# Optimization experiments

Hardware: AMD Instinct MI355X
Metric: run time of the kernel (lower is better)

Reference implementation:

```python
import jax, jax.numpy as jnp
import numpy as np
import math

INC, OUTC, NPARAM = 64, 128, 8
B, D, H, W = 2, 12, 48, 48
BN_EPS = 1e-5


def _p_n(num_param):
    # replicates LDConv_3D._get_p_n kernel-point layout
    base = round(math.sqrt(num_param))
    dep = round(num_param ** (1.0 / 3.0))
    row = num_param // (base * dep)
    mod = num_param % (base * dep)
    z, x, y = np.meshgrid(np.arange(dep), np.arange(row), np.arange(base), indexing='ij')
    z, x, y = z.ravel(), x.ravel(), y.ravel()
    if mod > 0:
        mz, mx, my = np.meshgrid(np.arange(dep, dep + 1), np.arange(row, row + 1), np.arange(mod), indexing='ij')
        z = np.concatenate([z, mz.ravel()])
        x = np.concatenate([x, mx.ravel()])
        y = np.concatenate([y, my.ravel()])
    return (jnp.asarray(z, jnp.float32), jnp.asarray(x, jnp.float32), jnp.asarray(y, jnp.float32))


def _conv3d(x, w, stride, pad):
    return jax.lax.conv_general_dilated(x, w, window_strides=stride, padding=pad,
                                        dimension_numbers=('NCDHW', 'OIDHW', 'NCDHW'))


def setup_inputs() -> dict:
    key = jax.random.key(0)
    ks = jax.random.split(key, 5)
    x = jax.random.normal(ks[0], (B, INC, D, H, W), jnp.float32)
    w_p = jax.random.normal(ks[1], (3 * NPARAM, INC, 3, 3, 3), jnp.float32) * 0.01
    b_p = jax.random.normal(ks[2], (3 * NPARAM,), jnp.float32) * 0.01
    w_conv = jax.random.normal(ks[3], (OUTC, INC, NPARAM, 1, 1), jnp.float32) * (1.0 / math.sqrt(INC * NPARAM))
    gamma = jnp.ones((OUTC,), jnp.float32)
    beta = jnp.zeros((OUTC,), jnp.float32)
    return {'x': x, 'w_p': w_p, 'b_p': b_p, 'w_conv': w_conv, 'gamma': gamma, 'beta': beta}


def reference(x, w_p, b_p, w_conv, gamma, beta):
    b, c, d, h, w = x.shape
    N = NPARAM
    # learned offsets: (b, 3N, d, h, w)
    offset = _conv3d(x, w_p, (1, 1, 1), [(1, 1), (1, 1), (1, 1)]) + b_p[None, :, None, None, None]
    off = jnp.transpose(offset, (0, 2, 3, 4, 1))  # b d h w 3N
    oz, ox, oy = off[..., :N], off[..., N:2 * N], off[..., 2 * N:]
    pnz, pnx, pny = _p_n(N)
    # sampling positions p = p_0 + p_n + offset  (stride=1)
    pz = oz + jnp.arange(d, dtype=jnp.float32)[None, :, None, None, None] + pnz
    px = ox + jnp.arange(h, dtype=jnp.float32)[None, None, :, None, None] + pnx
    py = oy + jnp.arange(w, dtype=jnp.float32)[None, None, None, :, None] + pny
    # integer corner coords (detached floor, clamped)
    fz = jnp.floor(jax.lax.stop_gradient(pz))
    fx = jnp.floor(jax.lax.stop_gradient(px))
    fy = jnp.floor(jax.lax.stop_gradient(py))
    qltz = jnp.clip(fz, 0, d - 1)
    qltx = jnp.clip(fx, 0, h - 1)
    qlty = jnp.clip(fy, 0, w - 1)
    qrbz = jnp.clip(fz + 1, 0, d - 1)
    qrbx = jnp.clip(fx + 1, 0, h - 1)
    qrby = jnp.clip(fy + 1, 0, w - 1)
    # clamped continuous positions
    pzc = jnp.clip(pz, 0, d - 1)
    pxc = jnp.clip(px, 0, h - 1)
    pyc = jnp.clip(py, 0, w - 1)
    # trilinear weights for the 4 gathered corners (as in source)
    g_lt = (1 + (qltz - pzc)) * (1 + (qltx - pxc)) * (1 + (qlty - pyc))
    g_rb = (1 - (qrbz - pzc)) * (1 - (qrbx - pxc)) * (1 - (qrby - pyc))
    g_lb = (1 + (qltz - pzc)) * (1 - (qrbx - pxc)) * (1 + (qlty - pyc))
    g_rt = (1 - (qrbz - pzc)) * (1 + (qltx - pxc)) * (1 - (qrby - pyc))
    x_flat = x.reshape(b, c, d * h * w)
    def gath(qz, qx, qy):
        idx = (qz.astype(jnp.int32) * (h * w) + qx.astype(jnp.int32) * w + qy.astype(jnp.int32)).reshape(b, -1)
        g = jax.vmap(lambda xf, i: jnp.take(xf, i, axis=1))(x_flat, idx)
        return g.reshape(b, c, d, h, w, N)
    x_lt = gath(qltz, qltx, qlty)
    x_rb = gath(qrbz, qrbx, qrby)
    x_lb = gath(qltz, qrbx, qlty)
    x_rt = gath(qrbz, qltx, qrby)
    x_off = (g_lt[:, None] * x_lt + g_rb[:, None] * x_rb +
             g_lb[:, None] * x_lb + g_rt[:, None] * x_rt)  # b c d h w N
    # rearrange 'b c d h w n -> b c (d n) h w'
    x_off = jnp.transpose(x_off, (0, 1, 2, 5, 3, 4)).reshape(b, c, d * N, h, w)
    out = _conv3d(x_off, w_conv, (N, 1, 1), [(0, 0), (0, 0), (0, 0)])  # b outc d h w
    # BatchNorm3d (training-mode batch stats, biased var) + SiLU
    mean = jnp.mean(out, axis=(0, 2, 3, 4), keepdims=True)
    var = jnp.mean((out - mean) ** 2, axis=(0, 2, 3, 4), keepdims=True)
    out = (out - mean) * jax.lax.rsqrt(var + BN_EPS)
    out = out * gamma[None, :, None, None, None] + beta[None, :, None, None, None]
    return jax.nn.silu(out)
```

## Files before the change

### kernel.cpp

```cpp
#include <hip/hip_runtime.h>
#include <math.h>

#define BATCH 2
#define INC   64
#define OUTCH 128
#define NP    8
#define DD    12
#define HH    48
#define WW    48
#define HW    (HH*WW)
#define DHW   (DD*HW)
#define SPTS  (BATCH*DHW)
#define KDIM  (INC*NP)
#define NELEM (BATCH*OUTCH*DHW)
#define VSTRIDE 520

#define WS_W2B  0
#define WS_W3   32768
#define WS_PART 88064
#define WS_XT   90112
#define WS_OFF  1859584

typedef __attribute__((ext_vector_type(8))) short short8;
typedef __attribute__((ext_vector_type(4))) float floatx4;

__device__ __forceinline__ ushort f2bf(float f) {
    unsigned u = __float_as_uint(f);
    unsigned r = (u + 0x7fffu + ((u >> 16) & 1u)) >> 16;
    return (ushort)r;
}

__device__ __forceinline__ unsigned interp2(unsigned a, unsigned b, unsigned c, unsigned d,
                                            float g0, float g1, float g2, float g3) {
    float vl = g0 * __uint_as_float(a << 16) + g1 * __uint_as_float(b << 16)
             + g2 * __uint_as_float(c << 16) + g3 * __uint_as_float(d << 16);
    float vh = g0 * __uint_as_float(a & 0xffff0000u) + g1 * __uint_as_float(b & 0xffff0000u)
             + g2 * __uint_as_float(c & 0xffff0000u) + g3 * __uint_as_float(d & 0xffff0000u);
    return (unsigned)f2bf(vl) | ((unsigned)f2bf(vh) << 16);
}

__global__ __launch_bounds__(256) void k_prep_w2b(const float* __restrict__ wc,
                                                  ushort* __restrict__ w2b) {
    int t = blockIdx.x * 256 + threadIdx.x;
    int j  = t & 7;
    int oc = (t >> 3) & 127;
    int kq = t >> 10;
    int e  = kq * 8 + j;
    int ic = e & 63;
    int n  = e >> 6;
    w2b[t] = f2bf(wc[(oc * INC + ic) * NP + n]);
}

__global__ __launch_bounds__(256) void k_prep_w3(const float* __restrict__ wp,
                                                 float* __restrict__ w3c) {
    int t = blockIdx.x * 256 + threadIdx.x;
    int ch = t & 31;
    int iu = t >> 5;
    w3c[t] = (ch < 24) ? wp[ch * 1728 + iu] : 0.f;
}

__global__ __launch_bounds__(256) void k_transpose_x(const float* __restrict__ x,
                                                     unsigned* __restrict__ xTu) {
    int t = blockIdx.x * 256 + threadIdx.x;
    int icp = t & 31;
    int sg  = t >> 5;
    int b   = sg / DHW;
    int s   = sg - b * DHW;
    const float* xb = x + (size_t)b * INC * DHW + s;
    float v0 = xb[(2 * icp) * DHW];
    float v1 = xb[(2 * icp + 1) * DHW];
    xTu[t] = (unsigned)f2bf(v0) | ((unsigned)f2bf(v1) << 16);
}

__global__ __launch_bounds__(256, 4) void k_conv(const float* __restrict__ x,
                                                 const float* __restrict__ w3c,
                                                 const float* __restrict__ bp,
                                                 float* __restrict__ off) {
    int t    = threadIdx.x;
    int lane = t & 63;
    int hgq  = __builtin_amdgcn_readfirstlane(t >> 6);
    int q0 = blockIdx.x * 128;
    int bb = q0 / DHW;
    int s0 = q0 - bb * DHW;
    int dp = s0 / HW;
    int rp = s0 - dp * HW + 2 * lane;
    int hp = rp / WW;
    int c0 = rp - hp * WW;
    const float* xb = x + (size_t)bb * INC * DHW;
    const float* wbase = w3c + hgq * 6;

    int rAo = (hp > 0      ? hp - 1 : 0     ) * WW;
    int rMo = hp * WW;
    int rBo = (hp < HH - 1 ? hp + 1 : HH - 1) * WW;
    int oL = (c0 > 0)  ? c0 - 2 : 0;
    int oM = c0;
    int oR = (c0 < 46) ? c0 + 2 : 46;

    float rm0 = (hp > 0)      ? 1.f : 0.f;
    float rm2 = (hp < HH - 1) ? 1.f : 0.f;
    float clm = (c0 > 0)      ? 1.f : 0.f;
    float crm = (c0 < 46)     ? 1.f : 0.f;
    float m0[9], m1[9];
    #pragma unroll
    for (int kx = 0; kx < 3; ++kx) {
        float rmv = kx == 0 ? rm0 : (kx == 1 ? 1.f : rm2);
        #pragma unroll
        for (int ky = 0; ky < 3; ++ky) {
            int u = kx * 3 + ky;
            m0[u] = rmv * (ky == 0 ? clm : 1.f);
            m1[u] = rmv * (ky == 2 ? crm : 1.f);
        }
    }

    float acc[2][6];
    #pragma unroll
    for (int c = 0; c < 6; ++c) { acc[0][c] = bp[hgq * 6 + c]; acc[1][c] = bp[hgq * 6 + c]; }

    #pragma unroll 1
    for (int kz = 0; kz < 3; ++kz) {
        int z = dp + kz - 1;
        if ((unsigned)z >= DD) continue;
        const float* xz = xb + z * HW;
        #pragma unroll 2
        for (int ic = 0; ic < 64; ++ic) {
            const float* xp = xz + (size_t)ic * DHW;
            float2 LA = *reinterpret_cast<const float2*>(xp + rAo + oL);
            float2 MA = *reinterpret_cast<const float2*>(xp + rAo + oM);
            float2 RA = *reinterpret_cast<const float2*>(xp + rAo + oR);
            float2 LM = *reinterpret_cast<const float2*>(xp + rMo + oL);
            float2 MM = *reinterpret_cast<const float2*>(xp + rMo + oM);
            float2 RM = *reinterpret_cast<const float2*>(xp + rMo + oR);
            float2 LB = *reinterpret_cast<const float2*>(xp + rBo + oL);
            float2 MB = *reinterpret_cast<const float2*>(xp + rBo + oM);
            float2 RB = *reinterpret_cast<const float2*>(xp + rBo + oR);
            const float* wk = wbase + (ic * 27 + kz * 9) * 32;
            #pragma unroll
            for (int kx = 0; kx < 3; ++kx) {
                float tv[4];
                if (kx == 0)      { tv[0] = LA.y; tv[1] = MA.x; tv[2] = MA.y; tv[3] = RA.x; }
                else if (kx == 1) { tv[0] = LM.y; tv[1] = MM.x; tv[2] = MM.y; tv[3] = RM.x; }
                else              { tv[0] = LB.y; tv[1] = MB.x; tv[2] = MB.y; tv[3] = RB.x; }
                #pragma unroll
                for (int ky = 0; ky < 3; ++ky) {
                    int u = kx * 3 + ky;
                    const float* w6 = wk + u * 32;
                    float xv0 = tv[ky]     * m0[u];
                    float xv1 = tv[ky + 1] * m1[u];
                    #pragma unroll
                    for (int c = 0; c < 6; ++c) {
                        acc[0][c] = fmaf(xv0, w6[c], acc[0][c]);
                        acc[1][c] = fmaf(xv1, w6[c], acc[1][c]);
                    }
                }
            }
        }
    }

    float2* o0 = reinterpret_cast<float2*>(off + (size_t)(q0 + 2 * lane) * 24 + hgq * 6);
    o0[0] = make_float2(acc[0][0], acc[0][1]);
    o0[1] = make_float2(acc[0][2], acc[0][3]);
    o0[2] = make_float2(acc[0][4], acc[0][5]);
    float2* o1 = reinterpret_cast<float2*>(off + (size_t)(q0 + 2 * lane + 1) * 24 + hgq * 6);
    o1[0] = make_float2(acc[1][0], acc[1][1]);
    o1[1] = make_float2(acc[1][2], acc[1][3]);
    o1[2] = make_float2(acc[1][4], acc[1][5]);
}

__global__ __launch_bounds__(256, 4) void k_fused(const unsigned* __restrict__ xTu,
                                                  const float* __restrict__ off,
                                                  const ushort* __restrict__ w2b,
                                                  float* __restrict__ out) {
    __shared__ __align__(16) ushort sVb[32 * VSTRIDE];
    __shared__ int   sMi[4][256];
    __shared__ float sMg[4][256];
    __shared__ __align__(16) unsigned stgBuf[64 * 36];

    int t  = threadIdx.x;
    int q0 = blockIdx.x * 32;
    int bb = q0 / DHW;

    {
        int i = t >> 3, n = t & 7;
        int s = q0 + i - bb * DHW;
        int d = s / HW; int r = s - d * HW; int h = r / WW; int w = r - h * WW;

        const float* op = off + (size_t)(q0 + i) * 24;
        float a0 = op[n];
        float a1 = op[8 + n];
        float a2 = op[16 + n];

        float pnz = (n < 6) ? (float)(n / 3) : 2.f;
        float pnx = (n < 6) ? 0.f : 1.f;
        float pny = (n < 6) ? (float)(n % 3) : (float)(n - 6);
        float pz = a0 + (float)d + pnz;
        float px = a1 + (float)h + pnx;
        float py = a2 + (float)w + pny;
        float fz = floorf(pz), fx = floorf(px), fy = floorf(py);
        float z0 = fminf(fmaxf(fz, 0.f), DD - 1.f), z1 = fminf(fmaxf(fz + 1.f, 0.f), DD - 1.f);
        float x0 = fminf(fmaxf(fx, 0.f), HH - 1.f), x1 = fminf(fmaxf(fx + 1.f, 0.f), HH - 1.f);
        float y0 = fminf(fmaxf(fy, 0.f), WW - 1.f), y1 = fminf(fmaxf(fy + 1.f, 0.f), WW - 1.f);
        float pzc = fminf(fmaxf(pz, 0.f), DD - 1.f);
        float pxc = fminf(fmaxf(px, 0.f), HH - 1.f);
        float pyc = fminf(fmaxf(py, 0.f), WW - 1.f);
        float wz0 = 1.f + z0 - pzc, wz1 = 1.f - z1 + pzc;
        float wx0 = 1.f + x0 - pxc, wx1 = 1.f - x1 + pxc;
        float wy0 = 1.f + y0 - pyc, wy1 = 1.f - y1 + pyc;
        float c0 = wz0 * wy0, c1 = wz1 * wy1;
        int iz0 = (int)z0, iz1 = (int)z1, ix0 = (int)x0, ix1 = (int)x1, iy0 = (int)y0, iy1 = (int)y1;
        sMi[0][t] = (iz0 * HH + ix0) * WW + iy0;
        sMi[1][t] = (iz0 * HH + ix1) * WW + iy0;
        sMi[2][t] = (iz1 * HH + ix0) * WW + iy1;
        sMi[3][t] = (iz1 * HH + ix1) * WW + iy1;
        sMg[0][t] = c0 * wx0;
        sMg[1][t] = c0 * wx1;
        sMg[2][t] = c1 * wx0;
        sMg[3][t] = c1 * wx1;
    }
    __syncthreads();

    {
        const unsigned* xTb = xTu + (size_t)bb * DHW * 32;
        unsigned* sVbU = reinterpret_cast<unsigned*>(sVb);
        int c  = t >> 3, o = t & 7;
        int tk = t >> 4, chq = t & 15;

        #pragma unroll 1
        for (int cc = 0; cc < 16; ++cc) {
            #pragma unroll
            for (int r2 = 0; r2 < 2; ++r2) {
                int cl  = r2 * 32 + c;
                int gt  = cc * 16 + (cl >> 2);
                int cid = cl & 3;
                int idx = sMi[cid][gt];
                uint4 v = reinterpret_cast<const uint4*>(xTb + (size_t)idx * 32)[o];
                *reinterpret_cast<uint4*>(&stgBuf[cl * 36 + o * 4]) = v;
            }
            __syncthreads();
            {
                int gt = cc * 16 + tk;
                float g0 = sMg[0][gt], g1 = sMg[1][gt], g2 = sMg[2][gt], g3 = sMg[3][gt];
                uint2 A = *reinterpret_cast<const uint2*>(&stgBuf[(tk * 4 + 0) * 36 + chq * 2]);
                uint2 B = *reinterpret_cast<const uint2*>(&stgBuf[(tk * 4 + 1) * 36 + chq * 2]);
                uint2 C = *reinterpret_cast<const uint2*>(&stgBuf[(tk * 4 + 2) * 36 + chq * 2]);
                uint2 D = *reinterpret_cast<const uint2*>(&stgBuf[(tk * 4 + 3) * 36 + chq * 2]);
                unsigned o0 = interp2(A.x, B.x, C.x, D.x, g0, g1, g2, g3);
                unsigned o1 = interp2(A.y, B.y, C.y, D.y, g0, g1, g2, g3);
                int ii = gt >> 3, nn = gt & 7;
                int wb = ii * (VSTRIDE / 2) + nn * 32 + chq * 2;
                sVbU[wb]     = o0;
                sVbU[wb + 1] = o1;
            }
            __syncthreads();
        }
    }

    {
        int lane = t & 63;
        int wid  = t >> 6;
        int l16  = lane & 15;
        int q    = lane >> 4;
        int ocA0 = (wid * 2) * 16 + l16;
        const ushort* A0 = w2b + ((q * 128) + ocA0) * 8;
        const ushort* A1 = A0 + 16 * 8;
        const ushort* B0 = sVb + l16 * VSTRIDE + q * 8;
        const ushort* B1 = B0 + 16 * VSTRIDE;

        floatx4 c00 = {0.f, 0.f, 0.f, 0.f};
        floatx4 c01 = {0.f, 0.f, 0.f, 0.f};
        floatx4 c10 = {0.f, 0.f, 0.f, 0.f};
        floatx4 c11 = {0.f, 0.f, 0.f, 0.f};

        #pragma unroll 4
        for (int kt = 0; kt < 16; ++kt) {
            short8 af0 = *reinterpret_cast<const short8*>(A0 + kt * 4096);
            short8 af1 = *reinterpret_cast<const short8*>(A1 + kt * 4096);
            short8 bf0 = *reinterpret_cast<const short8*>(B0 + kt * 32);
            short8 bf1 = *reinterpret_cast<const short8*>(B1 + kt * 32);
            c00 = __builtin_amdgcn_mfma_f32_16x16x32_bf16(af0, bf0, c00, 0, 0, 0);
            c01 = __builtin_amdgcn_mfma_f32_16x16x32_bf16(af0, bf1, c01, 0, 0, 0);
            c10 = __builtin_amdgcn_mfma_f32_16x16x32_bf16(af1, bf0, c10, 0, 0, 0);
            c11 = __builtin_amdgcn_mfma_f32_16x16x32_bf16(af1, bf1, c11, 0, 0, 0);
        }

        int s0 = q0 - bb * DHW;
        float* outb = out + (size_t)bb * OUTCH * DHW + s0;
        int ocRow = (wid * 2) * 16 + q * 4;
        #pragma unroll
        for (int rg = 0; rg < 4; ++rg) {
            outb[(ocRow + rg) * DHW + l16]            = c00[rg];
            outb[(ocRow + rg) * DHW + 16 + l16]       = c01[rg];
            outb[(ocRow + 16 + rg) * DHW + l16]       = c10[rg];
            outb[(ocRow + 16 + rg) * DHW + 16 + l16]  = c11[rg];
        }
    }
}

__global__ __launch_bounds__(256) void k_stats_partial(const float* __restrict__ out,
                                                       float* __restrict__ part) {
    int c = blockIdx.x >> 3;
    int j = blockIdx.x & 7;
    int b = j & 1, quarter = j >> 1;
    const float4* p = reinterpret_cast<const float4*>(
        out + (size_t)(b * OUTCH + c) * DHW + quarter * (DHW / 4));
    float sum = 0.f, ss = 0.f;
    for (int s = threadIdx.x; s < DHW / 16; s += 256) {
        float4 v = p[s];
        sum += v.x + v.y + v.z + v.w;
        ss = fmaf(v.x, v.x, ss); ss = fmaf(v.y, v.y, ss);
        ss = fmaf(v.z, v.z, ss); ss = fmaf(v.w, v.w, ss);
    }
    __shared__ float r1[256], r2[256];
    r1[threadIdx.x] = sum; r2[threadIdx.x] = ss;
    __syncthreads();
    for (int ofs = 128; ofs > 0; ofs >>= 1) {
        if (threadIdx.x < ofs) {
            r1[threadIdx.x] += r1[threadIdx.x + ofs];
            r2[threadIdx.x] += r2[threadIdx.x + ofs];
        }
        __syncthreads();
    }
    if (threadIdx.x == 0) {
        part[c * 8 + j]             = r1[0];
        part[OUTCH * 8 + c * 8 + j] = r2[0];
    }
}

__global__ __launch_bounds__(256) void k_bn_silu(float* __restrict__ out,
                                                 const float* __restrict__ part,
                                                 const float* __restrict__ gamma,
                                                 const float* __restrict__ beta) {
    int t = blockIdx.x * 256 + threadIdx.x;
    int base = t * 4;
    int c = (base / DHW) & 127;
    float sum = 0.f, ss = 0.f;
    #pragma unroll
    for (int j = 0; j < 8; ++j) {
        sum += part[c * 8 + j];
        ss  += part[OUTCH * 8 + c * 8 + j];
    }
    const float inv_n = 1.f / (float)(BATCH * DHW);
    float mean = sum * inv_n;
    float var  = ss * inv_n - mean * mean;
    float sc   = gamma[c] * rsqrtf(var + 1e-5f);
    float bi   = beta[c] - mean * sc;
    float4 v = *reinterpret_cast<float4*>(&out[base]);
    float y0 = fmaf(v.x, sc, bi);
    float y1 = fmaf(v.y, sc, bi);
    float y2 = fmaf(v.z, sc, bi);
    float y3 = fmaf(v.w, sc, bi);
    v.x = y0 / (1.f + expf(-y0));
    v.y = y1 / (1.f + expf(-y1));
    v.z = y2 / (1.f + expf(-y2));
    v.w = y3 / (1.f + expf(-y3));
    *reinterpret_cast<float4*>(&out[base]) = v;
}

extern "C" void kernel_launch(void* const* d_in, const int* in_sizes, int n_in,
                              void* d_out, int out_size, void* d_ws, size_t ws_size,
                              hipStream_t stream) {
    const float* x     = (const float*)d_in[0];
    const float* wp    = (const float*)d_in[1];
    const float* bp    = (const float*)d_in[2];
    const float* wc    = (const float*)d_in[3];
    const float* gamma = (const float*)d_in[4];
    const float* beta  = (const float*)d_in[5];
    float* out = (float*)d_out;
    float* ws  = (float*)d_ws;

    ushort*   w2b  = reinterpret_cast<ushort*>(ws + WS_W2B);
    float*    w3c  = ws + WS_W3;
    float*    part = ws + WS_PART;
    unsigned* xTu  = reinterpret_cast<unsigned*>(ws + WS_XT);
    float*    off  = ws + WS_OFF;

    k_prep_w2b<<<65536 / 256, 256, 0, stream>>>(wc, w2b);
    k_prep_w3<<<55296 / 256, 256, 0, stream>>>(wp, w3c);
    k_conv<<<SPTS / 128, 256, 0, stream>>>(x, w3c, bp, off);
    k_transpose_x<<<(SPTS * 32) / 256, 256, 0, stream>>>(x, xTu);
    k_fused<<<SPTS / 32, 256, 0, stream>>>(xTu, off, w2b, out);
    k_stats_partial<<<OUTCH * 8, 256, 0, stream>>>(out, part);
    k_bn_silu<<<(NELEM / 4) / 256, 256, 0, stream>>>(out, part, gamma, beta);
}
```

Measured before the change: 257.8 us.

## Transpose input to channel-last fp32 for offset conv and vectorize channel loads

A single transpose kernel now writes both a channel-last fp32 copy of x (placed in the output buffer as scratch) and the packed bf16 copy used by the fused kernel. The offset conv reads four channels at a time with float4 loads from the channel-last layout instead of strided per-channel float2 loads, and its launch bound is relaxed to 2 blocks per CU. The aim is fewer, wider memory transactions in the offset conv. In exchange the transpose writes more data, the conv can no longer overlap the transpose, and the larger per-thread register tile may lower occupancy.

```diff
diff --git a/kernel.cpp b/kernel.cpp
--- a/kernel.cpp
+++ b/kernel.cpp
@@ -59,20 +59,20 @@
     w3c[t] = (ch < 24) ? wp[ch * 1728 + iu] : 0.f;
 }
 
-__global__ __launch_bounds__(256) void k_transpose_x(const float* __restrict__ x,
-                                                     unsigned* __restrict__ xTu) {
-    int t = blockIdx.x * 256 + threadIdx.x;
-    int icp = t & 31;
-    int sg  = t >> 5;
-    int b   = sg / DHW;
-    int s   = sg - b * DHW;
-    const float* xb = x + (size_t)b * INC * DHW + s;
-    float v0 = xb[(2 * icp) * DHW];
-    float v1 = xb[(2 * icp + 1) * DHW];
-    xTu[t] = (unsigned)f2bf(v0) | ((unsigned)f2bf(v1) << 16);
-}
-
-__global__ __launch_bounds__(256, 4) void k_conv(const float* __restrict__ x,
+__global__ __launch_bounds__(256) void k_transpose_both(const float* __restrict__ x,
+                                                        float* __restrict__ xT32,
+                                                        ushort* __restrict__ xTuS) {
+    int t  = blockIdx.x * 256 + threadIdx.x;
+    int ic = t & 63;
+    int sg = t >> 6;
+    int b  = sg / DHW;
+    int s  = sg - b * DHW;
+    float v = x[((size_t)b * INC + ic) * DHW + s];
+    xT32[(size_t)sg * 64 + ic] = v;
+    xTuS[(size_t)sg * 64 + ic] = f2bf(v);
+}
+
+__global__ __launch_bounds__(256, 2) void k_conv(const float* __restrict__ xT32,
                                                  const float* __restrict__ w3c,
                                                  const float* __restrict__ bp,
                                                  float* __restrict__ off) {
@@ -86,15 +86,25 @@
     int rp = s0 - dp * HW + 2 * lane;
     int hp = rp / WW;
     int c0 = rp - hp * WW;
-    const float* xb = x + (size_t)bb * INC * DHW;
+    const float* xb = xT32 + (size_t)bb * DHW * 64;
     const float* wbase = w3c + hgq * 6;
 
-    int rAo = (hp > 0      ? hp - 1 : 0     ) * WW;
-    int rMo = hp * WW;
-    int rBo = (hp < HH - 1 ? hp + 1 : HH - 1) * WW;
-    int oL = (c0 > 0)  ? c0 - 2 : 0;
-    int oM = c0;
-    int oR = (c0 < 46) ? c0 + 2 : 46;
+    int rA = (hp > 0      ? hp - 1 : 0     );
+    int rM = hp;
+    int rB = (hp < HH - 1 ? hp + 1 : HH - 1);
+    int cl = (c0 > 0)  ? c0 - 1 : 0;
+    int cr = (c0 < 46) ? c0 + 2 : 47;
+    int hwOff[12];
+    {
+        int rows[3] = { rA, rM, rB };
+        #pragma unroll
+        for (int r = 0; r < 3; ++r) {
+            hwOff[r * 4 + 0] = (rows[r] * WW + cl)     * 64;
+            hwOff[r * 4 + 1] = (rows[r] * WW + c0)     * 64;
+            hwOff[r * 4 + 2] = (rows[r] * WW + c0 + 1) * 64;
+            hwOff[r * 4 + 3] = (rows[r] * WW + cr)     * 64;
+        }
+    }
 
     float rm0 = (hp > 0)      ? 1.f : 0.f;
     float rm2 = (hp < HH - 1) ? 1.f : 0.f;
@@ -120,36 +130,32 @@
     for (int kz = 0; kz < 3; ++kz) {
         int z = dp + kz - 1;
         if ((unsigned)z >= DD) continue;
-        const float* xz = xb + z * HW;
-        #pragma unroll 2
-        for (int ic = 0; ic < 64; ++ic) {
-            const float* xp = xz + (size_t)ic * DHW;
-            float2 LA = *reinterpret_cast<const float2*>(xp + rAo + oL);
-            float2 MA = *reinterpret_cast<const float2*>(xp + rAo + oM);
-            float2 RA = *reinterpret_cast<const float2*>(xp + rAo + oR);
-            float2 LM = *reinterpret_cast<const float2*>(xp + rMo + oL);
-            float2 MM = *reinterpret_cast<const float2*>(xp + rMo + oM);
-            float2 RM = *reinterpret_cast<const float2*>(xp + rMo + oR);
-            float2 LB = *reinterpret_cast<const float2*>(xp + rBo + oL);
-            float2 MB = *reinterpret_cast<const float2*>(xp + rBo + oM);
-            float2 RB = *reinterpret_cast<const float2*>(xp + rBo + oR);
-            const float* wk = wbase + (ic * 27 + kz * 9) * 32;
+        const float* xz = xb + (size_t)z * HW * 64;
+        #pragma unroll 1
+        for (int j = 0; j < 16; ++j) {
+            float4 T[12];
             #pragma unroll
-            for (int kx = 0; kx < 3; ++kx) {
-                float tv[4];
-                if (kx == 0)      { tv[0] = LA.y; tv[1] = MA.x; tv[2] = MA.y; tv[3] = RA.x; }
-                else if (kx == 1) { tv[0] = LM.y; tv[1] = MM.x; tv[2] = MM.y; tv[3] = RM.x; }
-                else              { tv[0] = LB.y; tv[1] = MB.x; tv[2] = MB.y; tv[3] = RB.x; }
+            for (int i = 0; i < 12; ++i)
+                T[i] = *reinterpret_cast<const float4*>(xz + hwOff[i] + j * 4);
+            #pragma unroll
+            for (int ii = 0; ii < 4; ++ii) {
+                int ic = j * 4 + ii;
+                const float* wk = wbase + (ic * 27 + kz * 9) * 32;
                 #pragma unroll
-                for (int ky = 0; ky < 3; ++ky) {
-                    int u = kx * 3 + ky;
-                    const float* w6 = wk + u * 32;
-                    float xv0 = tv[ky]     * m0[u];
-                    float xv1 = tv[ky + 1] * m1[u];
+                for (int kx = 0; kx < 3; ++kx) {
                     #pragma unroll
-                    for (int c = 0; c < 6; ++c) {
-                        acc[0][c] = fmaf(xv0, w6[c], acc[0][c]);
-                        acc[1][c] = fmaf(xv1, w6[c], acc[1][c]);
+                    for (int ky = 0; ky < 3; ++ky) {
+                        int u = kx * 3 + ky;
+                        const float* w6 = wk + u * 32;
+                        float tv0 = (ii == 0) ? T[kx*4+ky].x   : (ii == 1) ? T[kx*4+ky].y   : (ii == 2) ? T[kx*4+ky].z   : T[kx*4+ky].w;
+                        float tv1 = (ii == 0) ? T[kx*4+ky+1].x : (ii == 1) ? T[kx*4+ky+1].y : (ii == 2) ? T[kx*4+ky+1].z : T[kx*4+ky+1].w;
+                        float xv0 = tv0 * m0[u];
+                        float xv1 = tv1 * m1[u];
+                        #pragma unroll
+                        for (int c = 0; c < 6; ++c) {
+                            acc[0][c] = fmaf(xv0, w6[c], acc[0][c]);
+                            acc[1][c] = fmaf(xv1, w6[c], acc[1][c]);
+                        }
                     }
                 }
             }
@@ -372,11 +378,13 @@
     float*    part = ws + WS_PART;
     unsigned* xTu  = reinterpret_cast<unsigned*>(ws + WS_XT);
     float*    off  = ws + WS_OFF;
+    float*    xT32 = out;
 
     k_prep_w2b<<<65536 / 256, 256, 0, stream>>>(wc, w2b);
     k_prep_w3<<<55296 / 256, 256, 0, stream>>>(wp, w3c);
-    k_conv<<<SPTS / 128, 256, 0, stream>>>(x, w3c, bp, off);
-    k_transpose_x<<<(SPTS * 32) / 256, 256, 0, stream>>>(x, xTu);
+    k_transpose_both<<<(SPTS * 64) / 256, 256, 0, stream>>>(x, xT32,
+                                                            reinterpret_cast<ushort*>(xTu));
+    k_conv<<<SPTS / 128, 256, 0, stream>>>(xT32, w3c, bp, off);
     k_fused<<<SPTS / 32, 256, 0, stream>>>(xTu, off, w2b, out);
     k_stats_partial<<<OUTCH * 8, 256, 0, stream>>>(out, part);
     k_bn_silu<<<(NELEM / 4) / 256, 256, 0, stream>>>(out, part, gamma, beta);
```

Result: slower. 293.7 us (+13.9%).

## Gather corner samples directly into registers instead of staging through LDS

Applied to the files above, without the earlier changes.

Replaces the staged two-barrier gather loop, which copied corner rows into a shared staging buffer and then read them back to interpolate, with a loop where each thread loads its four corner uint4 vectors from global memory and interpolates 8 channels in registers. Per-point indices are packed as ushort4 and weights as float4 in shared memory. The VSTRIDE padding shrinks to 516 to reduce LDS footprint and shift the bank mapping. This removes 32 block barriers and the staging traffic, and frees LDS that could raise occupancy. The cost is that each thread issues more independent global loads, and the uint2 stores into the V tile may hit different bank conflicts.

```diff
diff --git a/kernel.cpp b/kernel.cpp
--- a/kernel.cpp
+++ b/kernel.cpp
@@ -13,7 +13,7 @@
 #define SPTS  (BATCH*DHW)
 #define KDIM  (INC*NP)
 #define NELEM (BATCH*OUTCH*DHW)
-#define VSTRIDE 520
+#define VSTRIDE 516
 
 #define WS_W2B  0
 #define WS_W3   32768
@@ -171,9 +171,8 @@
                                                   const ushort* __restrict__ w2b,
                                                   float* __restrict__ out) {
     __shared__ __align__(16) ushort sVb[32 * VSTRIDE];
-    __shared__ int   sMi[4][256];
-    __shared__ float sMg[4][256];
-    __shared__ __align__(16) unsigned stgBuf[64 * 36];
+    __shared__ __align__(16) ushort4 sMiP[256];
+    __shared__ __align__(16) float4  sMgP[256];
 
     int t  = threadIdx.x;
     int q0 = blockIdx.x * 32;
@@ -207,52 +206,40 @@
         float wy0 = 1.f + y0 - pyc, wy1 = 1.f - y1 + pyc;
         float c0 = wz0 * wy0, c1 = wz1 * wy1;
         int iz0 = (int)z0, iz1 = (int)z1, ix0 = (int)x0, ix1 = (int)x1, iy0 = (int)y0, iy1 = (int)y1;
-        sMi[0][t] = (iz0 * HH + ix0) * WW + iy0;
-        sMi[1][t] = (iz0 * HH + ix1) * WW + iy0;
-        sMi[2][t] = (iz1 * HH + ix0) * WW + iy1;
-        sMi[3][t] = (iz1 * HH + ix1) * WW + iy1;
-        sMg[0][t] = c0 * wx0;
-        sMg[1][t] = c0 * wx1;
-        sMg[2][t] = c1 * wx0;
-        sMg[3][t] = c1 * wx1;
+        ushort i0 = (ushort)((iz0 * HH + ix0) * WW + iy0);
+        ushort i1 = (ushort)((iz0 * HH + ix1) * WW + iy0);
+        ushort i2 = (ushort)((iz1 * HH + ix0) * WW + iy1);
+        ushort i3 = (ushort)((iz1 * HH + ix1) * WW + iy1);
+        sMiP[t] = make_ushort4(i0, i1, i2, i3);
+        sMgP[t] = make_float4(c0 * wx0, c0 * wx1, c1 * wx0, c1 * wx1);
     }
     __syncthreads();
 
     {
         const unsigned* xTb = xTu + (size_t)bb * DHW * 32;
         unsigned* sVbU = reinterpret_cast<unsigned*>(sVb);
-        int c  = t >> 3, o = t & 7;
-        int tk = t >> 4, chq = t & 15;
-
-        #pragma unroll 1
-        for (int cc = 0; cc < 16; ++cc) {
-            #pragma unroll
-            for (int r2 = 0; r2 < 2; ++r2) {
-                int cl  = r2 * 32 + c;
-                int gt  = cc * 16 + (cl >> 2);
-                int cid = cl & 3;
-                int idx = sMi[cid][gt];
-                uint4 v = reinterpret_cast<const uint4*>(xTb + (size_t)idx * 32)[o];
-                *reinterpret_cast<uint4*>(&stgBuf[cl * 36 + o * 4]) = v;
-            }
-            __syncthreads();
-            {
-                int gt = cc * 16 + tk;
-                float g0 = sMg[0][gt], g1 = sMg[1][gt], g2 = sMg[2][gt], g3 = sMg[3][gt];
-                uint2 A = *reinterpret_cast<const uint2*>(&stgBuf[(tk * 4 + 0) * 36 + chq * 2]);
-                uint2 B = *reinterpret_cast<const uint2*>(&stgBuf[(tk * 4 + 1) * 36 + chq * 2]);
-                uint2 C = *reinterpret_cast<const uint2*>(&stgBuf[(tk * 4 + 2) * 36 + chq * 2]);
-                uint2 D = *reinterpret_cast<const uint2*>(&stgBuf[(tk * 4 + 3) * 36 + chq * 2]);
-                unsigned o0 = interp2(A.x, B.x, C.x, D.x, g0, g1, g2, g3);
-                unsigned o1 = interp2(A.y, B.y, C.y, D.y, g0, g1, g2, g3);
-                int ii = gt >> 3, nn = gt & 7;
-                int wb = ii * (VSTRIDE / 2) + nn * 32 + chq * 2;
-                sVbU[wb]     = o0;
-                sVbU[wb + 1] = o1;
-            }
-            __syncthreads();
-        }
-    }
+        int tk = t >> 3, ch8 = t & 7;
+
+        #pragma unroll 4
+        for (int cc = 0; cc < 8; ++cc) {
+            int gt = cc * 32 + tk;
+            ushort4 mi = sMiP[gt];
+            float4  mg = sMgP[gt];
+            uint4 A = *reinterpret_cast<const uint4*>(xTb + (size_t)mi.x * 32 + ch8 * 4);
+            uint4 B = *reinterpret_cast<const uint4*>(xTb + (size_t)mi.y * 32 + ch8 * 4);
+            uint4 C = *reinterpret_cast<const uint4*>(xTb + (size_t)mi.z * 32 + ch8 * 4);
+            uint4 D = *reinterpret_cast<const uint4*>(xTb + (size_t)mi.w * 32 + ch8 * 4);
+            unsigned o0 = interp2(A.x, B.x, C.x, D.x, mg.x, mg.y, mg.z, mg.w);
+            unsigned o1 = interp2(A.y, B.y, C.y, D.y, mg.x, mg.y, mg.z, mg.w);
+            unsigned o2 = interp2(A.z, B.z, C.z, D.z, mg.x, mg.y, mg.z, mg.w);
+            unsigned o3 = interp2(A.w, B.w, C.w, D.w, mg.x, mg.y, mg.z, mg.w);
+            int ii = gt >> 3, nn = gt & 7;
+            int wb = ii * (VSTRIDE / 2) + nn * 32 + ch8 * 4;
+            *reinterpret_cast<uint2*>(&sVbU[wb])     = make_uint2(o0, o1);
+            *reinterpret_cast<uint2*>(&sVbU[wb + 2]) = make_uint2(o2, o3);
+        }
+    }
+    __syncthreads();
 
     {
         int lane = t & 63;
```

Result: faster. 249.5 us (-3.3%).
